# Optimization experiments

Hardware: AMD Instinct MI355X
Metric: run time of the kernel (lower is better)

The kernel has to match this reference:

```python
import jax, jax.numpy as jnp
import numpy as np

# All unordered pairs of 6 ligand sites (octahedral complex)
PAIRS = np.array([(i, j) for i in range(6) for j in range(i + 1, 6)], dtype=np.int32)  # [15, 2]

B, N_LIGS, D = 32768, 6, 64
IN_DIM = D + 2 * D  # core + lig_i + lig_j = 192
H1, H2 = 64, 32


def setup_inputs() -> dict:
    key = jax.random.key(0)
    ks = jax.random.split(key, 8)
    s = 0.05  # small init scale for numerical sanity
    return {
        "core": jax.random.normal(ks[0], (B, D), dtype=jnp.float32),
        "ligs": jax.random.normal(ks[1], (B, N_LIGS, D), dtype=jnp.float32),
        "W1": jax.random.normal(ks[2], (IN_DIM, H1), dtype=jnp.float32) * s,
        "b1": jnp.zeros((H1,), dtype=jnp.float32),
        "W2": jax.random.normal(ks[3], (H1, H2), dtype=jnp.float32) * s,
        "b2": jnp.zeros((H2,), dtype=jnp.float32),
        "W3": jax.random.normal(ks[4], (H2, 1), dtype=jnp.float32) * s,
        "b3": jnp.zeros((1,), dtype=jnp.float32),
    }


def _mlp(x, W1, b1, W2, b2, W3, b3):
    # Dense(softplus) -> Dense(softplus) -> Dense(1, linear); dropout is identity at inference
    h = jax.nn.softplus(x @ W1 + b1)
    h = jax.nn.softplus(h @ W2 + b2)
    return h @ W3 + b3  # [..., 1]


def reference(core, ligs, W1, b1, W2, b2, W3, b3):
    i_idx = jnp.asarray(PAIRS[:, 0])
    j_idx = jnp.asarray(PAIRS[:, 1])
    P = PAIRS.shape[0]
    li = ligs[:, i_idx, :]  # [B, P, D]
    lj = ligs[:, j_idx, :]  # [B, P, D]
    c = jnp.broadcast_to(core[:, None, :], (core.shape[0], P, core.shape[1]))
    x1 = jnp.concatenate([c, li, lj], axis=-1)  # [B, P, 3D]
    x2 = jnp.concatenate([c, lj, li], axis=-1)  # [B, P, 3D]
    res = 0.5 * (_mlp(x1, W1, b1, W2, b2, W3, b3) + _mlp(x2, W1, b1, W2, b2, W3, b3))  # [B, P, 1]
    return jnp.sum(res, axis=1)  # [B, 1]
```

## Files before the change

### kernel.cpp

```cpp
#include <hip/hip_runtime.h>
#include <hip/hip_fp16.h>
#include <stdint.h>


typedef __attribute__((ext_vector_type(8))) _Float16 f16x8;
typedef __attribute__((ext_vector_type(2))) __fp16   fp16v2;
typedef __attribute__((ext_vector_type(4))) float    f32x4;
typedef __attribute__((ext_vector_type(4))) unsigned int u32x4;

constexpr int   BPB       = 32;
constexpr int   NT        = 1024;
constexpr int   T_STRIDE  = 1664;
constexpr int   WT_OFF    = BPB * T_STRIDE;
constexpr int   Y_OFF     = WT_OFF + 192 * 128;
constexpr int   LDS_BYTES = Y_OFF + 128;

constexpr float L2E = 1.4426950408889634f;
constexpr float LN2 = 0.6931471805599453f;

constexpr unsigned long long I_BITS =
  (0ull<<0)|(0ull<<3)|(0ull<<6)|(0ull<<9)|(0ull<<12)|
  (1ull<<15)|(1ull<<18)|(1ull<<21)|(1ull<<24)|
  (2ull<<27)|(2ull<<30)|(2ull<<33)|
  (3ull<<36)|(3ull<<39)|(4ull<<42);
constexpr unsigned long long J_BITS =
  (1ull<<0)|(2ull<<3)|(3ull<<6)|(4ull<<9)|(5ull<<12)|
  (2ull<<15)|(3ull<<18)|(4ull<<21)|(5ull<<24)|
  (3ull<<27)|(4ull<<30)|(5ull<<33)|
  (4ull<<36)|(5ull<<39)|(5ull<<42);

__device__ __forceinline__ float sp2(float s) {
  float t = __builtin_amdgcn_exp2f(s);
  return __builtin_amdgcn_logf(1.0f + t);
}

__device__ __forceinline__ __half2 h1pair(__half2 u, __half2 a, __half2 b,
                                          __half2 one2) {
  __half2 s = __hadd2(__hadd2(u, a), b);
  __half2 t = h2exp2(s);
  return h2log2(__hadd2(one2, t));
}

__global__ __launch_bounds__(NT, 8)
void tb_fused(const float* __restrict__ core, const float* __restrict__ ligs,
              const float* __restrict__ W1,   const float* __restrict__ b1,
              const float* __restrict__ W2,   const float* __restrict__ b2,
              const float* __restrict__ W3,   const float* __restrict__ b3,
              float* __restrict__ out)
{
  extern __shared__ char smem[];
  const int tid  = (int)threadIdx.x;
  const int lane = tid & 63;
  const int ln   = lane & 15;
  const int qd   = lane >> 4;
  const int swz  = ln & 7;
  const int wv   = __builtin_amdgcn_readfirstlane(tid >> 6);
  const int b0   = (int)blockIdx.x * BPB;

  float* yred = (float*)(smem + Y_OFF);

  const int xr = wv >> 1;
  const int mt = wv & 1;
  float4 fA[4];
  if (wv < 14) {
    const float* src = (xr == 0)
        ? (core + (size_t)(b0 + mt * 16 + ln) * 64)
        : (ligs + ((size_t)(b0 + mt * 16 + ln) * 6 + (size_t)(xr - 1)) * 64);
    #pragma unroll
    for (int ks = 0; ks < 2; ++ks) {
      fA[ks * 2 + 0] = *(const float4*)(src + ks * 32 + qd * 8);
      fA[ks * 2 + 1] = *(const float4*)(src + ks * 32 + qd * 8 + 4);
    }
  }

  #pragma unroll
  for (int rep = 0; rep < 6; ++rep) {
    const int t  = tid + rep * NT;
    const int n  = t & 63;
    const int d0 = (t >> 6) << 1;
    const float g0 = W1[(size_t)d0 * 64 + n] * L2E;
    const float g1 = W1[(size_t)(d0 + 1) * 64 + n] * L2E;
    const uint32_t pk = (uint32_t)__half_as_ushort(__float2half(g0))
                      | ((uint32_t)__half_as_ushort(__float2half(g1)) << 16);
    const int slab = d0 >> 6, dl = d0 & 63;
    *(uint32_t*)(smem + WT_OFF + (slab * 64 + n) * 128
                 + (((dl >> 3) ^ (n & 7)) << 4) + (dl & 7) * 2) = pk;
  }
  if (tid < BPB) yred[tid] = 0.0f;
  __syncthreads();

  if (wv < 14) {
    union AF { f16x8 v; fp16v2 p[4]; } Afr[2];
    #pragma unroll
    for (int ks = 0; ks < 2; ++ks) {
      Afr[ks].p[0] = __builtin_amdgcn_cvt_pkrtz(fA[ks*2].x, fA[ks*2].y);
      Afr[ks].p[1] = __builtin_amdgcn_cvt_pkrtz(fA[ks*2].z, fA[ks*2].w);
      Afr[ks].p[2] = __builtin_amdgcn_cvt_pkrtz(fA[ks*2+1].x, fA[ks*2+1].y);
      Afr[ks].p[3] = __builtin_amdgcn_cvt_pkrtz(fA[ks*2+1].z, fA[ks*2+1].w);
    }

    const int sl_lo = (xr == 0) ? 0 : 1;
    const int sl_hi = (xr == 0) ? 0 : 2;
    #pragma unroll 1
    for (int sl = sl_lo; sl <= sl_hi; ++sl) {
      const int trow = (xr == 0) ? 0 : ((sl == 1) ? xr : 6 + xr);
      #pragma unroll
      for (int nt = 0; nt < 4; ++nt) {
        f32x4 c = {0.f, 0.f, 0.f, 0.f};
        #pragma unroll
        for (int ks = 0; ks < 2; ++ks) {
          const f16x8 Bf = *(const f16x8*)(smem + WT_OFF
              + (sl * 64 + nt * 16 + ln) * 128 + ((((ks << 2) + qd) ^ swz) << 4));
          c = __builtin_amdgcn_mfma_f32_16x16x32_f16(Afr[ks].v, Bf, c, 0, 0, 0);
        }
        const float bias = (trow == 0) ? b1[nt * 16 + ln] * L2E : 0.0f;
        #pragma unroll
        for (int reg = 0; reg < 4; ++reg) {
          const int b = mt * 16 + qd * 4 + reg;
          *(uint16_t*)(smem + (size_t)b * T_STRIDE + trow * 128
              + ((((nt << 1) + (ln >> 3)) ^ (b & 7)) << 4) + (ln & 7) * 2) =
              __half_as_ushort(__float2half(c[reg] + bias));
        }
      }
    }
  }

  f16x8 W2f[2][2];
  #pragma unroll
  for (int nt = 0; nt < 2; ++nt) {
    #pragma unroll
    for (int ks = 0; ks < 2; ++ks) {
      union { f16x8 v; uint16_t u[8]; } w;
      #pragma unroll
      for (int j = 0; j < 8; ++j)
        w.u[j] = __half_as_ushort(__float2half(
            W2[(size_t)(ks * 32 + qd * 8 + j) * 32 + nt * 16 + ln]));
      W2f[nt][ks] = w.v;
    }
  }
  float b2v[2], w3v[2];
  #pragma unroll
  for (int nt = 0; nt < 2; ++nt) {
    b2v[nt] = b2[nt * 16 + ln] * L2E;
    w3v[nt] = W3[nt * 16 + ln] * LN2;
  }

  __syncthreads();

  const int mtw = wv & 1;
  const int qr  = wv >> 1;
  const __half2 one2 = __float2half2_rn(1.0f);
  const char* Tb = smem + (size_t)(mtw * 16 + ln) * T_STRIDE;
  const int k0 = ((qd)     ^ swz) << 4;
  const int k1 = ((qd + 4) ^ swz) << 4;

  float yacc[4] = {0.f, 0.f, 0.f, 0.f};

  #pragma unroll 2
  for (int t3 = 0; t3 < 4; ++t3) {
    const int q = qr + 8 * t3;
    if (q >= 30) break;
    const int p  = q >> 1;
    const int iv = (int)((I_BITS >> (3 * p)) & 7ull);
    const int jv = (int)((J_BITS >> (3 * p)) & 7ull);
    const int An = (q & 1) ? jv : iv;
    const int Bn = (q & 1) ? iv : jv;
    const char* TA = Tb + (1 + An) * 128;
    const char* TB = Tb + (7 + Bn) * 128;

    union U4 { u32x4 u; __half2 h[4]; };
    U4 du0, da0, db0, du1, da1, db1;
    du0.u = *(const u32x4*)(Tb + k0);
    da0.u = *(const u32x4*)(TA + k0);
    db0.u = *(const u32x4*)(TB + k0);
    du1.u = *(const u32x4*)(Tb + k1);
    da1.u = *(const u32x4*)(TA + k1);
    db1.u = *(const u32x4*)(TB + k1);

    union { f16x8 v; __half2 h[4]; } A0, A1;
    #pragma unroll
    for (int w = 0; w < 4; ++w) A0.h[w] = h1pair(du0.h[w], da0.h[w], db0.h[w], one2);
    #pragma unroll
    for (int w = 0; w < 4; ++w) A1.h[w] = h1pair(du1.h[w], da1.h[w], db1.h[w], one2);

    f32x4 c0 = {0.f, 0.f, 0.f, 0.f};
    f32x4 c1 = {0.f, 0.f, 0.f, 0.f};
    c0 = __builtin_amdgcn_mfma_f32_16x16x32_f16(A0.v, W2f[0][0], c0, 0, 0, 0);
    c0 = __builtin_amdgcn_mfma_f32_16x16x32_f16(A1.v, W2f[0][1], c0, 0, 0, 0);
    c1 = __builtin_amdgcn_mfma_f32_16x16x32_f16(A0.v, W2f[1][0], c1, 0, 0, 0);
    c1 = __builtin_amdgcn_mfma_f32_16x16x32_f16(A1.v, W2f[1][1], c1, 0, 0, 0);

    #pragma unroll
    for (int reg = 0; reg < 4; ++reg) {
      yacc[reg] += sp2(c0[reg] + b2v[0]) * w3v[0]
                 + sp2(c1[reg] + b2v[1]) * w3v[1];
    }
  }

  #pragma unroll
  for (int reg = 0; reg < 4; ++reg) {
    float v = yacc[reg];
    v += __shfl_xor(v, 1);
    v += __shfl_xor(v, 2);
    v += __shfl_xor(v, 4);
    v += __shfl_xor(v, 8);
    yacc[reg] = v;
  }
  if (ln == 0) {
    #pragma unroll
    for (int reg = 0; reg < 4; ++reg)
      atomicAdd(&yred[mtw * 16 + qd * 4 + reg], yacc[reg]);
  }
  __syncthreads();
  if (tid < BPB) out[b0 + tid] = 0.5f * yred[tid] + 15.0f * b3[0];
}

extern "C" void kernel_launch(void* const* d_in, const int* in_sizes, int n_in,
                              void* d_out, int out_size, void* d_ws, size_t ws_size,
                              hipStream_t stream) {
  (void)d_ws; (void)ws_size;
  const float* core = (const float*)d_in[0];
  const float* ligs = (const float*)d_in[1];
  const float* W1   = (const float*)d_in[2];
  const float* b1   = (const float*)d_in[3];
  const float* W2   = (const float*)d_in[4];
  const float* b2   = (const float*)d_in[5];
  const float* W3   = (const float*)d_in[6];
  const float* b3   = (const float*)d_in[7];
  float* out = (float*)d_out;

  const int B = in_sizes[0] / 64;
  const int grid = B / BPB;

  (void)hipFuncSetAttribute((const void*)tb_fused,
                            hipFuncAttributeMaxDynamicSharedMemorySize, LDS_BYTES);
  tb_fused<<<dim3(grid), dim3(NT), LDS_BYTES, stream>>>(
      core, ligs, W1, b1, W2, b2, W3, b3, out);
}
```

Before: 127.4 us.

## Halve block size to 16 batch rows with 8 waves and rebalanced layer-1 work

Each block now handles 16 batch rows with 512 threads instead of 32 rows with 1024. Layer-1 work is redistributed so each of 8 waves handles one or two of the 13 projection tiles, with no idle waves. The core tile loads are hoisted out of the pair loop, and the b2 bias is folded into the MFMA accumulator init. The W1 staging into LDS now runs 12 reps per block and is repeated across twice as many blocks, which adds redundant weight traffic per batch row in exchange for smaller blocks and better wave utilization.

```diff
diff --git a/kernel.cpp b/kernel.cpp
--- a/kernel.cpp
+++ b/kernel.cpp
@@ -8,8 +8,8 @@
 typedef __attribute__((ext_vector_type(4))) float    f32x4;
 typedef __attribute__((ext_vector_type(4))) unsigned int u32x4;
 
-constexpr int   BPB       = 32;
-constexpr int   NT        = 1024;
+constexpr int   BPB       = 16;
+constexpr int   NT        = 512;
 constexpr int   T_STRIDE  = 1664;
 constexpr int   WT_OFF    = BPB * T_STRIDE;
 constexpr int   Y_OFF     = WT_OFF + 192 * 128;
@@ -41,7 +41,7 @@
   return h2log2(__hadd2(one2, t));
 }
 
-__global__ __launch_bounds__(NT, 8)
+__global__ __launch_bounds__(NT, 6)
 void tb_fused(const float* __restrict__ core, const float* __restrict__ ligs,
               const float* __restrict__ W1,   const float* __restrict__ b1,
               const float* __restrict__ W2,   const float* __restrict__ b2,
@@ -59,22 +59,34 @@
 
   float* yred = (float*)(smem + Y_OFF);
 
-  const int xr = wv >> 1;
-  const int mt = wv & 1;
-  float4 fA[4];
-  if (wv < 14) {
+  const int t1 = wv;
+  const int t2 = wv + 8;
+  const bool j2 = (t2 < 13);
+
+  float4 fA[2][4];
+  {
+    const int xr = (t1 == 0) ? 0 : (t1 <= 6 ? t1 : t1 - 6);
     const float* src = (xr == 0)
-        ? (core + (size_t)(b0 + mt * 16 + ln) * 64)
-        : (ligs + ((size_t)(b0 + mt * 16 + ln) * 6 + (size_t)(xr - 1)) * 64);
-    #pragma unroll
-    for (int ks = 0; ks < 2; ++ks) {
-      fA[ks * 2 + 0] = *(const float4*)(src + ks * 32 + qd * 8);
-      fA[ks * 2 + 1] = *(const float4*)(src + ks * 32 + qd * 8 + 4);
-    }
-  }
-
-  #pragma unroll
-  for (int rep = 0; rep < 6; ++rep) {
+        ? (core + (size_t)(b0 + ln) * 64)
+        : (ligs + ((size_t)(b0 + ln) * 6 + (size_t)(xr - 1)) * 64);
+    #pragma unroll
+    for (int ks = 0; ks < 2; ++ks) {
+      fA[0][ks * 2 + 0] = *(const float4*)(src + ks * 32 + qd * 8);
+      fA[0][ks * 2 + 1] = *(const float4*)(src + ks * 32 + qd * 8 + 4);
+    }
+  }
+  if (j2) {
+    const int xr = t2 - 6;
+    const float* src = ligs + ((size_t)(b0 + ln) * 6 + (size_t)(xr - 1)) * 64;
+    #pragma unroll
+    for (int ks = 0; ks < 2; ++ks) {
+      fA[1][ks * 2 + 0] = *(const float4*)(src + ks * 32 + qd * 8);
+      fA[1][ks * 2 + 1] = *(const float4*)(src + ks * 32 + qd * 8 + 4);
+    }
+  }
+
+  #pragma unroll
+  for (int rep = 0; rep < 12; ++rep) {
     const int t  = tid + rep * NT;
     const int n  = t & 63;
     const int d0 = (t >> 6) << 1;
@@ -86,41 +98,43 @@
     *(uint32_t*)(smem + WT_OFF + (slab * 64 + n) * 128
                  + (((dl >> 3) ^ (n & 7)) << 4) + (dl & 7) * 2) = pk;
   }
+
+  union AFr { f16x8 v; fp16v2 p[4]; } Afr[2][2];
+  #pragma unroll
+  for (int jj = 0; jj < 2; ++jj) {
+    if (jj == 1 && !j2) break;
+    #pragma unroll
+    for (int ks = 0; ks < 2; ++ks) {
+      Afr[jj][ks].p[0] = __builtin_amdgcn_cvt_pkrtz(fA[jj][ks*2].x, fA[jj][ks*2].y);
+      Afr[jj][ks].p[1] = __builtin_amdgcn_cvt_pkrtz(fA[jj][ks*2].z, fA[jj][ks*2].w);
+      Afr[jj][ks].p[2] = __builtin_amdgcn_cvt_pkrtz(fA[jj][ks*2+1].x, fA[jj][ks*2+1].y);
+      Afr[jj][ks].p[3] = __builtin_amdgcn_cvt_pkrtz(fA[jj][ks*2+1].z, fA[jj][ks*2+1].w);
+    }
+  }
   if (tid < BPB) yred[tid] = 0.0f;
   __syncthreads();
 
-  if (wv < 14) {
-    union AF { f16x8 v; fp16v2 p[4]; } Afr[2];
-    #pragma unroll
-    for (int ks = 0; ks < 2; ++ks) {
-      Afr[ks].p[0] = __builtin_amdgcn_cvt_pkrtz(fA[ks*2].x, fA[ks*2].y);
-      Afr[ks].p[1] = __builtin_amdgcn_cvt_pkrtz(fA[ks*2].z, fA[ks*2].w);
-      Afr[ks].p[2] = __builtin_amdgcn_cvt_pkrtz(fA[ks*2+1].x, fA[ks*2+1].y);
-      Afr[ks].p[3] = __builtin_amdgcn_cvt_pkrtz(fA[ks*2+1].z, fA[ks*2+1].w);
-    }
-
-    const int sl_lo = (xr == 0) ? 0 : 1;
-    const int sl_hi = (xr == 0) ? 0 : 2;
-    #pragma unroll 1
-    for (int sl = sl_lo; sl <= sl_hi; ++sl) {
-      const int trow = (xr == 0) ? 0 : ((sl == 1) ? xr : 6 + xr);
+  #pragma unroll
+  for (int jj = 0; jj < 2; ++jj) {
+    if (jj == 1 && !j2) break;
+    const int t  = (jj == 0) ? t1 : t2;
+    const int sl = (t == 0) ? 0 : (t <= 6 ? 1 : 2);
+    #pragma unroll
+    for (int nt = 0; nt < 4; ++nt) {
+      f32x4 c = {0.f, 0.f, 0.f, 0.f};
       #pragma unroll
-      for (int nt = 0; nt < 4; ++nt) {
-        f32x4 c = {0.f, 0.f, 0.f, 0.f};
-        #pragma unroll
-        for (int ks = 0; ks < 2; ++ks) {
-          const f16x8 Bf = *(const f16x8*)(smem + WT_OFF
-              + (sl * 64 + nt * 16 + ln) * 128 + ((((ks << 2) + qd) ^ swz) << 4));
-          c = __builtin_amdgcn_mfma_f32_16x16x32_f16(Afr[ks].v, Bf, c, 0, 0, 0);
-        }
-        const float bias = (trow == 0) ? b1[nt * 16 + ln] * L2E : 0.0f;
-        #pragma unroll
-        for (int reg = 0; reg < 4; ++reg) {
-          const int b = mt * 16 + qd * 4 + reg;
-          *(uint16_t*)(smem + (size_t)b * T_STRIDE + trow * 128
-              + ((((nt << 1) + (ln >> 3)) ^ (b & 7)) << 4) + (ln & 7) * 2) =
-              __half_as_ushort(__float2half(c[reg] + bias));
-        }
+      for (int ks = 0; ks < 2; ++ks) {
+        const f16x8 Bf = *(const f16x8*)(smem + WT_OFF
+            + (sl * 64 + nt * 16 + ln) * 128 + ((((ks << 2) + qd) ^ swz) << 4));
+        c = __builtin_amdgcn_mfma_f32_16x16x32_f16(Afr[jj][ks].v, Bf, c, 0, 0, 0);
+      }
+      const float bias = (t == 0) ? b1[nt * 16 + ln] * L2E : 0.0f;
+      #pragma unroll
+      for (int reg = 0; reg < 4; ++reg) {
+        const int b = qd * 4 + reg;
+        *(uint16_t*)(smem + (size_t)b * T_STRIDE + t * 128
+            + ((((nt << 1) + (ln >> 3)) ^ (b & 7)) << 4) + (ln & 7) * 2) =
+            __half_as_ushort(__float2half(c[reg] + bias));
       }
     }
   }
@@ -147,12 +161,17 @@
 
   __syncthreads();
 
-  const int mtw = wv & 1;
-  const int qr  = wv >> 1;
+  const int qr = wv;
   const __half2 one2 = __float2half2_rn(1.0f);
-  const char* Tb = smem + (size_t)(mtw * 16 + ln) * T_STRIDE;
+  const char* Tb = smem + (size_t)ln * T_STRIDE;
   const int k0 = ((qd)     ^ swz) << 4;
   const int k1 = ((qd + 4) ^ swz) << 4;
+
+  union U4 { u32x4 u; __half2 h[4]; };
+
+  U4 du0, du1;
+  du0.u = *(const u32x4*)(Tb + k0);
+  du1.u = *(const u32x4*)(Tb + k1);
 
   float yacc[4] = {0.f, 0.f, 0.f, 0.f};
 
@@ -168,12 +187,9 @@
     const char* TA = Tb + (1 + An) * 128;
     const char* TB = Tb + (7 + Bn) * 128;
 
-    union U4 { u32x4 u; __half2 h[4]; };
-    U4 du0, da0, db0, du1, da1, db1;
-    du0.u = *(const u32x4*)(Tb + k0);
+    U4 da0, db0, da1, db1;
     da0.u = *(const u32x4*)(TA + k0);
     db0.u = *(const u32x4*)(TB + k0);
-    du1.u = *(const u32x4*)(Tb + k1);
     da1.u = *(const u32x4*)(TA + k1);
     db1.u = *(const u32x4*)(TB + k1);
 
@@ -183,8 +199,8 @@
     #pragma unroll
     for (int w = 0; w < 4; ++w) A1.h[w] = h1pair(du1.h[w], da1.h[w], db1.h[w], one2);
 
-    f32x4 c0 = {0.f, 0.f, 0.f, 0.f};
-    f32x4 c1 = {0.f, 0.f, 0.f, 0.f};
+    f32x4 c0 = {b2v[0], b2v[0], b2v[0], b2v[0]};
+    f32x4 c1 = {b2v[1], b2v[1], b2v[1], b2v[1]};
     c0 = __builtin_amdgcn_mfma_f32_16x16x32_f16(A0.v, W2f[0][0], c0, 0, 0, 0);
     c0 = __builtin_amdgcn_mfma_f32_16x16x32_f16(A1.v, W2f[0][1], c0, 0, 0, 0);
     c1 = __builtin_amdgcn_mfma_f32_16x16x32_f16(A0.v, W2f[1][0], c1, 0, 0, 0);
@@ -192,8 +208,7 @@
 
     #pragma unroll
     for (int reg = 0; reg < 4; ++reg) {
-      yacc[reg] += sp2(c0[reg] + b2v[0]) * w3v[0]
-                 + sp2(c1[reg] + b2v[1]) * w3v[1];
+      yacc[reg] += sp2(c0[reg]) * w3v[0] + sp2(c1[reg]) * w3v[1];
     }
   }
 
@@ -209,7 +224,7 @@
   if (ln == 0) {
     #pragma unroll
     for (int reg = 0; reg < 4; ++reg)
-      atomicAdd(&yred[mtw * 16 + qd * 4 + reg], yacc[reg]);
+      atomicAdd(&yred[qd * 4 + reg], yacc[reg]);
   }
   __syncthreads();
   if (tid < BPB) out[b0 + tid] = 0.5f * yred[tid] + 15.0f * b3[0];
```

Measured after the change: 131.1 us. 1.03x slower.

## Precompute fp16 swizzled weights in prep kernel and transpose layer-1 MFMA output stores

Applied to the files above, without the earlier changes.

Adds a small prep kernel that converts W1, W2 and the biases to fp16 in their final swizzled or transposed layouts in workspace, once per call. Each block then copies W1 into LDS with uint4 loads instead of doing strided float loads plus conversion. Layer 1 swaps the MFMA operands so each lane can write a packed 8-byte vector of outputs instead of four scattered 2-byte stores. The biases are folded into the MFMA accumulator init, and the core row load is hoisted out of the pair loop. The cost is an extra kernel launch and a dependency on workspace contents.

```diff
diff --git a/kernel.cpp b/kernel.cpp
--- a/kernel.cpp
+++ b/kernel.cpp
@@ -14,6 +14,12 @@
 constexpr int   WT_OFF    = BPB * T_STRIDE;
 constexpr int   Y_OFF     = WT_OFF + 192 * 128;
 constexpr int   LDS_BYTES = Y_OFF + 128;
+
+constexpr int   WS_W1T   = 0;
+constexpr int   WS_W2T   = 24576;
+constexpr int   WS_B1    = 28672;
+constexpr int   WS_B2    = 28928;
+constexpr int   WS_W3    = 29056;
 
 constexpr float L2E = 1.4426950408889634f;
 constexpr float LN2 = 0.6931471805599453f;
@@ -41,11 +47,36 @@
   return h2log2(__hadd2(one2, t));
 }
 
+__global__ __launch_bounds__(256)
+void prep(const float* __restrict__ W1, const float* __restrict__ b1,
+          const float* __restrict__ W2, const float* __restrict__ b2,
+          const float* __restrict__ W3, char* __restrict__ ws)
+{
+  const int t = (int)(blockIdx.x * blockDim.x + threadIdx.x);
+  if (t < 12288) {
+    const int r = t >> 6, dl = t & 63;
+    const int slab = r >> 6, n = r & 63;
+    const int dg = slab * 64 + dl;
+    const float v = W1[(size_t)dg * 64 + n] * L2E;
+    *(uint16_t*)(ws + WS_W1T + r * 128 + (((dl >> 3) ^ (r & 7)) << 4)
+                 + (dl & 7) * 2) = __half_as_ushort(__float2half(v));
+  } else if (t < 14336) {
+    const int e = t - 12288;
+    const int k = e >> 5, m = e & 31;
+    *(uint16_t*)(ws + WS_W2T + (m * 64 + k) * 2) =
+        __half_as_ushort(__float2half(W2[e]));
+  } else if (t < 14400) {
+    ((float*)(ws + WS_B1))[t - 14336] = b1[t - 14336] * L2E;
+  } else if (t < 14432) {
+    ((float*)(ws + WS_B2))[t - 14400] = b2[t - 14400] * L2E;
+  } else if (t < 14464) {
+    ((float*)(ws + WS_W3))[t - 14432] = W3[t - 14432] * LN2;
+  }
+}
+
 __global__ __launch_bounds__(NT, 8)
 void tb_fused(const float* __restrict__ core, const float* __restrict__ ligs,
-              const float* __restrict__ W1,   const float* __restrict__ b1,
-              const float* __restrict__ W2,   const float* __restrict__ b2,
-              const float* __restrict__ W3,   const float* __restrict__ b3,
+              const char* __restrict__ ws,   const float* __restrict__ b3,
               float* __restrict__ out)
 {
   extern __shared__ char smem[];
@@ -73,30 +104,23 @@
     }
   }
 
-  #pragma unroll
-  for (int rep = 0; rep < 6; ++rep) {
-    const int t  = tid + rep * NT;
-    const int n  = t & 63;
-    const int d0 = (t >> 6) << 1;
-    const float g0 = W1[(size_t)d0 * 64 + n] * L2E;
-    const float g1 = W1[(size_t)(d0 + 1) * 64 + n] * L2E;
-    const uint32_t pk = (uint32_t)__half_as_ushort(__float2half(g0))
-                      | ((uint32_t)__half_as_ushort(__float2half(g1)) << 16);
-    const int slab = d0 >> 6, dl = d0 & 63;
-    *(uint32_t*)(smem + WT_OFF + (slab * 64 + n) * 128
-                 + (((dl >> 3) ^ (n & 7)) << 4) + (dl & 7) * 2) = pk;
+  {
+    const uint4* src = (const uint4*)(ws + WS_W1T);
+    uint4*       dst = (uint4*)(smem + WT_OFF);
+    dst[tid] = src[tid];
+    if (tid < 512) dst[1024 + tid] = src[1024 + tid];
   }
   if (tid < BPB) yred[tid] = 0.0f;
   __syncthreads();
 
   if (wv < 14) {
-    union AF { f16x8 v; fp16v2 p[4]; } Afr[2];
+    union AFr { f16x8 v; fp16v2 p[4]; } Xf[2];
     #pragma unroll
     for (int ks = 0; ks < 2; ++ks) {
-      Afr[ks].p[0] = __builtin_amdgcn_cvt_pkrtz(fA[ks*2].x, fA[ks*2].y);
-      Afr[ks].p[1] = __builtin_amdgcn_cvt_pkrtz(fA[ks*2].z, fA[ks*2].w);
-      Afr[ks].p[2] = __builtin_amdgcn_cvt_pkrtz(fA[ks*2+1].x, fA[ks*2+1].y);
-      Afr[ks].p[3] = __builtin_amdgcn_cvt_pkrtz(fA[ks*2+1].z, fA[ks*2+1].w);
+      Xf[ks].p[0] = __builtin_amdgcn_cvt_pkrtz(fA[ks*2].x, fA[ks*2].y);
+      Xf[ks].p[1] = __builtin_amdgcn_cvt_pkrtz(fA[ks*2].z, fA[ks*2].w);
+      Xf[ks].p[2] = __builtin_amdgcn_cvt_pkrtz(fA[ks*2+1].x, fA[ks*2+1].y);
+      Xf[ks].p[3] = __builtin_amdgcn_cvt_pkrtz(fA[ks*2+1].z, fA[ks*2+1].w);
     }
 
     const int sl_lo = (xr == 0) ? 0 : 1;
@@ -106,43 +130,39 @@
       const int trow = (xr == 0) ? 0 : ((sl == 1) ? xr : 6 + xr);
       #pragma unroll
       for (int nt = 0; nt < 4; ++nt) {
-        f32x4 c = {0.f, 0.f, 0.f, 0.f};
+        f32x4 c;
+        if (trow == 0) {
+          c = *(const f32x4*)(ws + WS_B1 + (nt * 16 + qd * 4) * 4);
+        } else {
+          c = (f32x4){0.f, 0.f, 0.f, 0.f};
+        }
         #pragma unroll
         for (int ks = 0; ks < 2; ++ks) {
-          const f16x8 Bf = *(const f16x8*)(smem + WT_OFF
+          const f16x8 Wf = *(const f16x8*)(smem + WT_OFF
               + (sl * 64 + nt * 16 + ln) * 128 + ((((ks << 2) + qd) ^ swz) << 4));
-          c = __builtin_amdgcn_mfma_f32_16x16x32_f16(Afr[ks].v, Bf, c, 0, 0, 0);
+          c = __builtin_amdgcn_mfma_f32_16x16x32_f16(Wf, Xf[ks].v, c, 0, 0, 0);
         }
-        const float bias = (trow == 0) ? b1[nt * 16 + ln] * L2E : 0.0f;
-        #pragma unroll
-        for (int reg = 0; reg < 4; ++reg) {
-          const int b = mt * 16 + qd * 4 + reg;
-          *(uint16_t*)(smem + (size_t)b * T_STRIDE + trow * 128
-              + ((((nt << 1) + (ln >> 3)) ^ (b & 7)) << 4) + (ln & 7) * 2) =
-              __half_as_ushort(__float2half(c[reg] + bias));
-        }
+        union PK { uint2 u; __half2 h[2]; } pk;
+        pk.h[0] = __halves2half2(__float2half(c[0]), __float2half(c[1]));
+        pk.h[1] = __halves2half2(__float2half(c[2]), __float2half(c[3]));
+        *(uint2*)(smem + (size_t)(mt * 16 + ln) * T_STRIDE + trow * 128
+                  + ((((nt << 1) + (qd >> 1)) ^ swz) << 4) + (qd & 1) * 8) = pk.u;
       }
     }
   }
 
   f16x8 W2f[2][2];
   #pragma unroll
-  for (int nt = 0; nt < 2; ++nt) {
-    #pragma unroll
-    for (int ks = 0; ks < 2; ++ks) {
-      union { f16x8 v; uint16_t u[8]; } w;
-      #pragma unroll
-      for (int j = 0; j < 8; ++j)
-        w.u[j] = __half_as_ushort(__float2half(
-            W2[(size_t)(ks * 32 + qd * 8 + j) * 32 + nt * 16 + ln]));
-      W2f[nt][ks] = w.v;
-    }
-  }
+  for (int nt = 0; nt < 2; ++nt)
+    #pragma unroll
+    for (int ks = 0; ks < 2; ++ks)
+      W2f[nt][ks] = *(const f16x8*)(ws + WS_W2T
+          + ((nt * 16 + ln) * 64 + ks * 32 + qd * 8) * 2);
   float b2v[2], w3v[2];
   #pragma unroll
   for (int nt = 0; nt < 2; ++nt) {
-    b2v[nt] = b2[nt * 16 + ln] * L2E;
-    w3v[nt] = W3[nt * 16 + ln] * LN2;
+    b2v[nt] = ((const float*)(ws + WS_B2))[nt * 16 + ln];
+    w3v[nt] = ((const float*)(ws + WS_W3))[nt * 16 + ln];
   }
 
   __syncthreads();
@@ -153,6 +173,12 @@
   const char* Tb = smem + (size_t)(mtw * 16 + ln) * T_STRIDE;
   const int k0 = ((qd)     ^ swz) << 4;
   const int k1 = ((qd + 4) ^ swz) << 4;
+
+  union U4 { u32x4 u; __half2 h[4]; };
+
+  U4 du0, du1;
+  du0.u = *(const u32x4*)(Tb + k0);
+  du1.u = *(const u32x4*)(Tb + k1);
 
   float yacc[4] = {0.f, 0.f, 0.f, 0.f};
 
@@ -168,12 +194,9 @@
     const char* TA = Tb + (1 + An) * 128;
     const char* TB = Tb + (7 + Bn) * 128;
 
-    union U4 { u32x4 u; __half2 h[4]; };
-    U4 du0, da0, db0, du1, da1, db1;
-    du0.u = *(const u32x4*)(Tb + k0);
+    U4 da0, db0, da1, db1;
     da0.u = *(const u32x4*)(TA + k0);
     db0.u = *(const u32x4*)(TB + k0);
-    du1.u = *(const u32x4*)(Tb + k1);
     da1.u = *(const u32x4*)(TA + k1);
     db1.u = *(const u32x4*)(TB + k1);
 
@@ -183,8 +206,8 @@
     #pragma unroll
     for (int w = 0; w < 4; ++w) A1.h[w] = h1pair(du1.h[w], da1.h[w], db1.h[w], one2);
 
-    f32x4 c0 = {0.f, 0.f, 0.f, 0.f};
-    f32x4 c1 = {0.f, 0.f, 0.f, 0.f};
+    f32x4 c0 = {b2v[0], b2v[0], b2v[0], b2v[0]};
+    f32x4 c1 = {b2v[1], b2v[1], b2v[1], b2v[1]};
     c0 = __builtin_amdgcn_mfma_f32_16x16x32_f16(A0.v, W2f[0][0], c0, 0, 0, 0);
     c0 = __builtin_amdgcn_mfma_f32_16x16x32_f16(A1.v, W2f[0][1], c0, 0, 0, 0);
     c1 = __builtin_amdgcn_mfma_f32_16x16x32_f16(A0.v, W2f[1][0], c1, 0, 0, 0);
@@ -192,8 +215,7 @@
 
     #pragma unroll
     for (int reg = 0; reg < 4; ++reg) {
-      yacc[reg] += sp2(c0[reg] + b2v[0]) * w3v[0]
-                 + sp2(c1[reg] + b2v[1]) * w3v[1];
+      yacc[reg] += sp2(c0[reg]) * w3v[0] + sp2(c1[reg]) * w3v[1];
     }
   }
 
@@ -218,7 +240,6 @@
 extern "C" void kernel_launch(void* const* d_in, const int* in_sizes, int n_in,
                               void* d_out, int out_size, void* d_ws, size_t ws_size,
                               hipStream_t stream) {
-  (void)d_ws; (void)ws_size;
   const float* core = (const float*)d_in[0];
   const float* ligs = (const float*)d_in[1];
   const float* W1   = (const float*)d_in[2];
@@ -228,12 +249,15 @@
   const float* W3   = (const float*)d_in[6];
   const float* b3   = (const float*)d_in[7];
   float* out = (float*)d_out;
+  char*  ws  = (char*)d_ws;
 
   const int B = in_sizes[0] / 64;
   const int grid = B / BPB;
+
+  prep<<<dim3(57), dim3(256), 0, stream>>>(W1, b1, W2, b2, W3, ws);
 
   (void)hipFuncSetAttribute((const void*)tb_fused,
                             hipFuncAttributeMaxDynamicSharedMemorySize, LDS_BYTES);
   tb_fused<<<dim3(grid), dim3(NT), LDS_BYTES, stream>>>(
-      core, ligs, W1, b1, W2, b2, W3, b3, out);
-}
+      core, ligs, ws, b3, out);
+}
```

After: 126.3 us, median of 2. About the same (-0.9%).
